# Optimization experiments

Hardware: AMD Instinct MI355X
Metric: run time of the kernel (lower is better)

Reference implementation:

```python
import jax, jax.numpy as jnp
import numpy as np

EPS = 1e-5

def _layer_norm(x, w):
    mu = jnp.mean(x, axis=-1, keepdims=True)
    var = jnp.mean(jnp.square(x - mu), axis=-1, keepdims=True)
    return (x - mu) * jax.lax.rsqrt(var + EPS) * w

def setup_inputs() -> dict:
    key = jax.random.key(0)
    ks = jax.random.split(key, 5)
    B, T, C, H = 2, 2048, 1024, 16
    std = 0.02
    return {
        "x": jax.random.normal(ks[0], (B, T, C), dtype=jnp.float32),
        "ln1_w": jnp.ones((C,), dtype=jnp.float32),
        "w_attn": jax.random.normal(ks[1], (C, 3 * C), dtype=jnp.float32) * std,
        "w_proj": jax.random.normal(ks[2], (C, C), dtype=jnp.float32) * std,
        "ln2_w": jnp.ones((C,), dtype=jnp.float32),
        "w_fc": jax.random.normal(ks[3], (C, 4 * C), dtype=jnp.float32) * std,
        "w_cproj": jax.random.normal(ks[4], (4 * C, C), dtype=jnp.float32) * std,
    }

def reference(x, ln1_w, w_attn, w_proj, ln2_w, w_fc, w_cproj):
    B, T, C = x.shape
    H = 16
    Dh = C // H
    # --- causal self-attention on ln1(x) ---
    h = _layer_norm(x, ln1_w)
    qkv = h @ w_attn                      # [B,T,3C]
    q, k, v = jnp.split(qkv, 3, axis=-1)
    # [B,T,C] -> [B,H,T,Dh]
    q = q.reshape(B, T, H, Dh).transpose(0, 2, 1, 3)
    k = k.reshape(B, T, H, Dh).transpose(0, 2, 1, 3)
    v = v.reshape(B, T, H, Dh).transpose(0, 2, 1, 3)
    # NOTE: original scales by full embed dim C**-0.5, not head_dim**-0.5
    scores = jnp.einsum('bhqd,bhkd->bhqk', q, k) * (C ** -0.5)
    causal = jnp.tril(jnp.ones((T, T), dtype=bool))
    scores = jnp.where(causal, scores, -jnp.inf)
    probs = jax.nn.softmax(scores, axis=-1)  # dropout=0.0 (eval)
    y = jnp.einsum('bhqk,bhkd->bhqd', probs, v)
    y = y.transpose(0, 2, 1, 3).reshape(B, T, C)
    x = x + y @ w_proj
    # --- MLP on ln2(x) ---
    h = _layer_norm(x, ln2_w)
    x = x + jax.nn.relu(h @ w_fc) @ w_cproj
    return x
```

## Files before the change

### kernel.cpp

```cpp
#include <hip/hip_runtime.h>

typedef __attribute__((ext_vector_type(8))) __bf16 bf16x8;
typedef __attribute__((ext_vector_type(4))) float f32x4;
typedef __attribute__((ext_vector_type(8))) unsigned short u16x8;
typedef __attribute__((ext_vector_type(4))) unsigned short u16x4;
typedef unsigned short u16;

__device__ __forceinline__ u16 f2bf(float f) {
  return __builtin_bit_cast(u16, (__bf16)f);
}
__device__ __forceinline__ float bf2f(u16 u) {
  return __builtin_bit_cast(float, ((unsigned)u) << 16);
}

__device__ __forceinline__ f32x4 mfma16(bf16x8 a, bf16x8 b, f32x4 c) {
  return __builtin_amdgcn_mfma_f32_16x16x32_bf16(a, b, c, 0, 0, 0);
}

__device__ __forceinline__ void gl_lds16(const void* g, void* l) {
  __builtin_amdgcn_global_load_lds(
      (const __attribute__((address_space(1))) unsigned int*)g,
      (__attribute__((address_space(3))) unsigned int*)l, 16, 0, 0);
}

__device__ __forceinline__ f32x4 fmax4(f32x4 a, f32x4 b) {
  f32x4 r;
  r[0] = fmaxf(a[0], b[0]); r[1] = fmaxf(a[1], b[1]);
  r[2] = fmaxf(a[2], b[2]); r[3] = fmaxf(a[3], b[3]);
  return r;
}

__global__ __launch_bounds__(256) void convT_all(const float* __restrict__ w0,
                                                 u16* __restrict__ o0,
                                                 const float* __restrict__ w1,
                                                 u16* __restrict__ o1,
                                                 const float* __restrict__ w2,
                                                 u16* __restrict__ o2) {
  __shared__ float tile[64][65];
  const int id = blockIdx.x;
  const float* in;
  u16* outT;
  int K, N, bx, by;
  if (id < 768) { in = w0; outT = o0; K = 1024; N = 3072; bx = id & 15; by = id >> 4; }
  else if (id < 1024) { const int j = id - 768; in = w1; outT = o1; K = 1024; N = 1024; bx = j & 15; by = j >> 4; }
  else { const int j = id - 1024; in = w2; outT = o2; K = 1024; N = 4096; bx = j & 15; by = j >> 4; }
  const int t = threadIdx.x;
  const int tk = bx * 64, tn = by * 64;
  const int lk = t >> 4, ln = (t & 15) * 4;
#pragma unroll
  for (int r = 0; r < 4; ++r) {
    const int k = lk + r * 16;
    const float4 v = *(const float4*)(in + (size_t)(tk + k) * N + tn + ln);
    tile[k][ln + 0] = v.x; tile[k][ln + 1] = v.y;
    tile[k][ln + 2] = v.z; tile[k][ln + 3] = v.w;
  }
  __syncthreads();
  const int sn = t >> 2, sk = (t & 3) * 4;
#pragma unroll
  for (int j = 0; j < 4; ++j) {
    const int k = sk + j * 16;
    ushort4 o;
    o.x = f2bf(tile[k + 0][sn]); o.y = f2bf(tile[k + 1][sn]);
    o.z = f2bf(tile[k + 2][sn]); o.w = f2bf(tile[k + 3][sn]);
    *(ushort4*)(outT + (size_t)(tn + sn) * K + tk + k) = o;
  }
}

__global__ __launch_bounds__(256) void convT(const float* __restrict__ in,
                                             u16* __restrict__ outT, int K, int N) {
  __shared__ float tile[64][65];
  const int t = threadIdx.x;
  const int tk = blockIdx.x * 64, tn = blockIdx.y * 64;
  const int lk = t >> 4, ln = (t & 15) * 4;
#pragma unroll
  for (int r = 0; r < 4; ++r) {
    const int k = lk + r * 16;
    const float4 v = *(const float4*)(in + (size_t)(tk + k) * N + tn + ln);
    tile[k][ln + 0] = v.x; tile[k][ln + 1] = v.y;
    tile[k][ln + 2] = v.z; tile[k][ln + 3] = v.w;
  }
  __syncthreads();
  const int sn = t >> 2, sk = (t & 3) * 4;
#pragma unroll
  for (int j = 0; j < 4; ++j) {
    const int k = sk + j * 16;
    ushort4 o;
    o.x = f2bf(tile[k + 0][sn]); o.y = f2bf(tile[k + 1][sn]);
    o.z = f2bf(tile[k + 2][sn]); o.w = f2bf(tile[k + 3][sn]);
    *(ushort4*)(outT + (size_t)(tn + sn) * K + tk + k) = o;
  }
}

__global__ __launch_bounds__(256) void vtrans(const u16* __restrict__ qkvb,
                                              u16* __restrict__ vT) {
  __shared__ u16 tile[64][72];
  const int t = threadIdx.x;
  const int tt0 = blockIdx.x * 64;
  const int bh = blockIdx.y;
  const int b = bh >> 4, h = bh & 15;
  const u16* src = qkvb + (size_t)(b * 2048 + tt0) * 3072 + 2048 + h * 64;
  {
    const int tl = t >> 2, d0 = (t & 3) * 16;
    const u16x8 a0 = *(const u16x8*)(src + (size_t)tl * 3072 + d0);
    const u16x8 a1 = *(const u16x8*)(src + (size_t)tl * 3072 + d0 + 8);
    *(u16x8*)(&tile[tl][d0]) = a0;
    *(u16x8*)(&tile[tl][d0 + 8]) = a1;
  }
  __syncthreads();
  {
    const int dh = t >> 2, t0 = (t & 3) * 16;
    u16x8 o0, o1;
#pragma unroll
    for (int jj = 0; jj < 8; ++jj) {
      o0[jj] = tile[t0 + jj][dh];
      o1[jj] = tile[t0 + 8 + jj][dh];
    }
    u16* dst = vT + ((size_t)bh * 64 + dh) * 2048 + tt0 + t0;
    *(u16x8*)dst = o0;
    *(u16x8*)(dst + 8) = o1;
  }
}

__global__ __launch_bounds__(256) void ln_bf16(const float* __restrict__ x,
                                               const float* __restrict__ wgt,
                                               u16* __restrict__ out) {
  const int row = blockIdx.x, t = threadIdx.x;
  const float4 v = ((const float4*)(x + (size_t)row * 1024))[t];
  float s = v.x + v.y + v.z + v.w;
  float q = v.x * v.x + v.y * v.y + v.z * v.z + v.w * v.w;
#pragma unroll
  for (int d = 32; d; d >>= 1) { s += __shfl_xor(s, d); q += __shfl_xor(q, d); }
  __shared__ float sb[8];
  const int wv = t >> 6;
  if ((t & 63) == 0) { sb[wv] = s; sb[4 + wv] = q; }
  __syncthreads();
  s = sb[0] + sb[1] + sb[2] + sb[3];
  q = sb[4] + sb[5] + sb[6] + sb[7];
  const float mu = s * (1.f / 1024.f);
  const float rstd = rsqrtf(q * (1.f / 1024.f) - mu * mu + 1e-5f);
  const float4 w4 = ((const float4*)wgt)[t];
  ushort4 o;
  o.x = f2bf((v.x - mu) * rstd * w4.x);
  o.y = f2bf((v.y - mu) * rstd * w4.y);
  o.z = f2bf((v.z - mu) * rstd * w4.z);
  o.w = f2bf((v.w - mu) * rstd * w4.w);
  *(ushort4*)(out + (size_t)row * 1024 + t * 4) = o;
}

__global__ __launch_bounds__(256) void reduce_ln(const float* __restrict__ x,
                                                 const u16* __restrict__ p, int nseg,
                                                 const float* __restrict__ wgt,
                                                 float* __restrict__ x1,
                                                 u16* __restrict__ h2) {
  const int row = blockIdx.x, t = threadIdx.x;
  const size_t ro = (size_t)row * 1024 + t * 4;
  float4 v = *(const float4*)(x + ro);
  for (int sgm = 0; sgm < nseg; ++sgm) {
    const ushort4 u = *(const ushort4*)(p + (size_t)sgm * 4096 * 1024 + ro);
    v.x += bf2f(u.x); v.y += bf2f(u.y); v.z += bf2f(u.z); v.w += bf2f(u.w);
  }
  *(float4*)(x1 + ro) = v;
  float s = v.x + v.y + v.z + v.w;
  float q = v.x * v.x + v.y * v.y + v.z * v.z + v.w * v.w;
#pragma unroll
  for (int d = 32; d; d >>= 1) { s += __shfl_xor(s, d); q += __shfl_xor(q, d); }
  __shared__ float sb[8];
  const int wv = t >> 6;
  if ((t & 63) == 0) { sb[wv] = s; sb[4 + wv] = q; }
  __syncthreads();
  s = sb[0] + sb[1] + sb[2] + sb[3];
  q = sb[4] + sb[5] + sb[6] + sb[7];
  const float mu = s * (1.f / 1024.f);
  const float rstd = rsqrtf(q * (1.f / 1024.f) - mu * mu + 1e-5f);
  const float4 w4 = ((const float4*)wgt)[t];
  ushort4 o;
  o.x = f2bf((v.x - mu) * rstd * w4.x);
  o.y = f2bf((v.y - mu) * rstd * w4.y);
  o.z = f2bf((v.z - mu) * rstd * w4.z);
  o.w = f2bf((v.w - mu) * rstd * w4.w);
  *(ushort4*)(h2 + ro) = o;
}

__global__ __launch_bounds__(256) void reduce_out(const float* __restrict__ x1,
                                                  const u16* __restrict__ p, int nseg,
                                                  float* __restrict__ out) {
  const int i = blockIdx.x * blockDim.x + threadIdx.x;
  const size_t ro = (size_t)i * 4;
  float4 v = *(const float4*)(x1 + ro);
  for (int sgm = 0; sgm < nseg; ++sgm) {
    const ushort4 u = *(const ushort4*)(p + (size_t)sgm * 4096 * 1024 + ro);
    v.x += bf2f(u.x); v.y += bf2f(u.y); v.z += bf2f(u.z); v.w += bf2f(u.w);
  }
  *(float4*)(out + ro) = v;
}

template <int EPI>
__global__ __launch_bounds__(256) void gemm128(const u16* __restrict__ A,
                                               const u16* __restrict__ Bt,
                                               void* __restrict__ outp,
                                               int M, int N, int K) {
  __shared__ u16 As[2][4096];
  __shared__ u16 Bs[2][4096];
  const unsigned gx = gridDim.x, gy = gridDim.y, gxy = gx * gy;
  const unsigned nwg = gxy * gridDim.z;
  unsigned f = (blockIdx.z * gy + blockIdx.y) * gx + blockIdx.x;
  if ((nwg & 7u) == 0u) { const unsigned qq = nwg >> 3; f = (f & 7u) * qq + (f >> 3); }
  const int bx = f % gx, by = (f / gx) % gy, bz = f / gxy;

  const int t = threadIdx.x, w = t >> 6, l = t & 63;
  const int lr = l & 15, g = l >> 4;
  const int row0 = by * 128, col0 = bx * 128;
  const int segK = K / gridDim.z;
  const int k0 = bz * segK, kend = k0 + segK;
  const int wr = w >> 1, wc = w & 1;
  f32x4 acc[4][4] = {};

  const int sr = t >> 2;
  const int sk = (((t & 3) ^ (sr & 3)) << 3);
  const u16* Ag = A + (size_t)(row0 + sr) * K + sk;
  const u16* Bg = Bt + (size_t)(col0 + sr) * K + sk;
  const size_t rstride = (size_t)64 * K;

  auto stage = [&](int kt, int bb) {
    u16* AsW = As[bb] + w * 512;
    u16* BsW = Bs[bb] + w * 512;
    gl_lds16(Ag + kt, AsW);
    gl_lds16(Ag + kt + rstride, AsW + 2048);
    gl_lds16(Bg + kt, BsW);
    gl_lds16(Bg + kt + rstride, BsW + 2048);
  };

  const int gsw = (g ^ (lr & 3)) * 8;

  stage(k0, 0);
  __syncthreads();
  int cur = 0;
  for (int kt = k0; kt < kend; kt += 32) {
    if (kt + 32 < kend) stage(kt + 32, cur ^ 1);
    bf16x8 af[4], bfr[4];
#pragma unroll
    for (int m = 0; m < 4; ++m)
      af[m] = *(const bf16x8*)(As[cur] + (wr * 64 + m * 16 + lr) * 32 + gsw);
#pragma unroll
    for (int n = 0; n < 4; ++n)
      bfr[n] = *(const bf16x8*)(Bs[cur] + (wc * 64 + n * 16 + lr) * 32 + gsw);
#pragma unroll
    for (int m = 0; m < 4; ++m)
#pragma unroll
      for (int n = 0; n < 4; ++n) acc[m][n] = mfma16(af[m], bfr[n], acc[m][n]);
    __syncthreads();
    cur ^= 1;
  }

  const size_t segoff = (size_t)bz * M * N;
#pragma unroll
  for (int m = 0; m < 4; ++m)
#pragma unroll
    for (int n = 0; n < 4; ++n)
#pragma unroll
      for (int r = 0; r < 4; ++r) {
        const int row = row0 + wr * 64 + m * 16 + g * 4 + r;
        const int col = col0 + wc * 64 + n * 16 + lr;
        const size_t idx = (size_t)row * N + col;
        const float v = acc[m][n][r];
        if constexpr (EPI == 0) ((u16*)outp)[idx] = f2bf(v);
        else if constexpr (EPI == 2) ((u16*)outp)[idx] = f2bf(fmaxf(v, 0.f));
        else ((u16*)outp)[segoff + idx] = f2bf(v);
      }
}

template <int EPI>
__global__ __launch_bounds__(512, 2) void gemm256(const u16* __restrict__ A,
                                                  const u16* __restrict__ Bt,
                                                  u16* __restrict__ outp,
                                                  int M, int N, int K) {
  __shared__ u16 S[2][32768];
  const unsigned gx = gridDim.x, gy = gridDim.y, gxy = gx * gy;
  const unsigned nwg = gxy * gridDim.z;
  unsigned f = (blockIdx.z * gy + blockIdx.y) * gx + blockIdx.x;
  if ((nwg & 7u) == 0u) { const unsigned qq = nwg >> 3; f = (f & 7u) * qq + (f >> 3); }
  const int bx = f % gx, by = (f / gx) % gy, bz = f / gxy;
  const int t = threadIdx.x, w = t >> 6, l = t & 63;
  const int lr = l & 15, g = l >> 4;
  const int wr = w >> 2, wc = w & 3;
  const int row0 = by * 256, col0 = bx * 256;
  const int segK = K / gridDim.z;
  const int k0 = bz * segK;
  const int NT = segK >> 6;

  f32x4 acc[8][4] = {};

  const int jr0 = t >> 2;
  const int jr1 = jr0 + 128;
  const int jks = ((t & 3) ^ (jr0 & 3)) << 3;
  auto stage_half = [&](int ht, int idx) {
    const int buf = ht & 1;
    u16* db = &S[buf][(idx & 1) * 16384 + (idx >> 1) * 8192 + w * 512];
    const u16* gb = (idx & 1) ? Bt : A;
    const int rc0 = (idx & 1) ? col0 : row0;
    const int kb = k0 + ht * 64 + (idx >> 1) * 32;
    gl_lds16(gb + (size_t)(rc0 + jr0) * K + kb + jks, db);
    gl_lds16(gb + (size_t)(rc0 + jr1) * K + kb + jks, db + 4096);
  };

  const int gsw = (g ^ (lr & 3)) * 8;

  stage_half(0, 0); stage_half(0, 1); stage_half(0, 2); stage_half(0, 3);
  stage_half(1, 0); stage_half(1, 1);
  asm volatile("s_waitcnt vmcnt(4)" ::: "memory");
  __builtin_amdgcn_s_barrier();

  for (int T = 0; T < NT; ++T) {
    const int cur = T & 1;
    const u16* Ab = &S[cur][0];
    const u16* Bb = &S[cur][16384];
    bf16x8 bfr[4];
#pragma unroll
    for (int sub = 0; sub < 4; ++sub) {
      const int mq = sub & 1, ks = sub >> 1;
      if (mq == 0) {
#pragma unroll
        for (int n = 0; n < 4; ++n)
          bfr[n] = *(const bf16x8*)(Bb + ks * 8192 + (wc * 64 + n * 16 + lr) * 32 + gsw);
      }
      bf16x8 af[4];
#pragma unroll
      for (int m = 0; m < 4; ++m)
        af[m] = *(const bf16x8*)(Ab + ks * 8192 +
                                 (wr * 128 + mq * 64 + m * 16 + lr) * 32 + gsw);
      if (sub < 2) { if (T + 1 < NT) stage_half(T + 1, 2 + sub); }
      else         { if (T + 2 < NT) stage_half(T + 2, sub - 2); }
      __builtin_amdgcn_s_barrier();
      __builtin_amdgcn_s_setprio(1);
#pragma unroll
      for (int m = 0; m < 4; ++m)
#pragma unroll
        for (int n = 0; n < 4; ++n)
          acc[mq * 4 + m][n] = mfma16(af[m], bfr[n], acc[mq * 4 + m][n]);
      __builtin_amdgcn_s_setprio(0);
      if (sub == 3) asm volatile("s_waitcnt vmcnt(4)" ::: "memory");
      __builtin_amdgcn_s_barrier();
    }
  }

  const size_t segoff = (size_t)bz * M * N;
#pragma unroll
  for (int m = 0; m < 8; ++m)
#pragma unroll
    for (int n = 0; n < 4; ++n)
#pragma unroll
      for (int r = 0; r < 4; ++r) {
        const int row = row0 + wr * 128 + m * 16 + g * 4 + r;
        const int col = col0 + wc * 64 + n * 16 + lr;
        const size_t idx = (size_t)row * N + col;
        const float v = acc[m][n][r];
        if constexpr (EPI == 0) outp[idx] = f2bf(v);
        else if constexpr (EPI == 2) outp[idx] = f2bf(fmaxf(v, 0.f));
        else outp[segoff + idx] = f2bf(v);
      }
}

__global__ __launch_bounds__(256) void attn_fwd(const u16* __restrict__ qkvb,
                                                const u16* __restrict__ vT,
                                                u16* __restrict__ y) {
  __shared__ u16 Ks[2][4096];
  __shared__ u16 Vs[2][4096];
  __shared__ u16 Pb[4][16 * 64];
  const int t = threadIdx.x, w = t >> 6, l = t & 63;
  const int lr = l & 15, g = l >> 4;
  const unsigned f = blockIdx.y * gridDim.x + blockIdx.x;
  const int xcd = f & 7, j = f >> 3;
  const int bh = xcd + 8 * (j & 3);
  const int qt = 31 - (j >> 2);
  const int b = bh >> 4, h = bh & 15;
  const size_t base = (size_t)b * 2048 * 3072;
  const u16* Kg = qkvb + base + 1024 + h * 64;
  const u16* Vg = vT + (size_t)bh * 64 * 2048;
  u16* Pw = &Pb[w][0];
  const int pkey = (lr & 7) << 3;
  const float SCL = 0.0450842200277855f;

  auto stageK = [&](int kv0, int bb) {
#pragma unroll
    for (int r = 0; r < 2; ++r) {
      const int dl = (r * 256 + t) * 16;
      const int row = dl >> 7;
      const int srcb = (dl & 127) ^ ((row & 7) << 4);
      gl_lds16(Kg + (size_t)(kv0 + row) * 3072 + (srcb >> 1),
               (char*)Ks[bb] + r * 4096 + w * 1024);
    }
  };
  auto stageV = [&](int kv0, int bb) {
#pragma unroll
    for (int r = 0; r < 2; ++r) {
      const int dl = (r * 256 + t) * 16;
      const int dh = dl >> 7;
      const int srcb = (dl & 127) ^ ((dh & 7) << 4);
      gl_lds16(Vg + (size_t)dh * 2048 + kv0 + (srcb >> 1),
               (char*)Vs[bb] + r * 4096 + w * 1024);
    }
  };

  const int q0w = qt * 64 + w * 16, nt = qt + 1;
  const u16* Qp = qkvb + base + (size_t)(q0w + lr) * 3072 + h * 64;
  const bf16x8 qf0 = *(const bf16x8*)(Qp + g * 8);
  const bf16x8 qf1 = *(const bf16x8*)(Qp + 32 + g * 8);
  f32x4 o[4] = {};
  float m1 = -1e30f, s1 = 0.f;

  stageK(0, 0);
  stageV(0, 0);
  __syncthreads();

  int ct = 0;
  for (int tt = 0; tt < nt; ++tt) {
    const int kv0 = tt * 64;
    if (tt + 1 < nt) {
      stageK(kv0 + 64, ct ^ 1);
      stageV(kv0 + 64, ct ^ 1);
    }

    const u16* Kbuf = Ks[ct];
    const u16* Vbuf = Vs[ct];
    f32x4 s4[4];
#pragma unroll
    for (int i = 0; i < 4; ++i) {
      const int row = i * 16 + lr;
      const int sw = (row & 7) << 4;
      const bf16x8 k0 = *(const bf16x8*)(Kbuf + row * 64 + (((g * 16) ^ sw) >> 1));
      const bf16x8 k1 = *(const bf16x8*)(Kbuf + row * 64 + (((64 + g * 16) ^ sw) >> 1));
      f32x4 z = {0.f, 0.f, 0.f, 0.f};
      z = mfma16(k0, qf0, z);
      s4[i] = mfma16(k1, qf1, z);
    }
    if (kv0 + 64 > q0w) {
#pragma unroll
      for (int i = 0; i < 4; ++i)
#pragma unroll
        for (int r = 0; r < 4; ++r)
          if (kv0 + i * 16 + g * 4 + r > q0w + lr) s4[i][r] = -1e30f;
    }
    const f32x4 mm = fmax4(fmax4(s4[0], s4[1]), fmax4(s4[2], s4[3]));
    float mx = fmaxf(fmaxf(mm[0], mm[1]), fmaxf(mm[2], mm[3]));
    mx = fmaxf(mx, __shfl_xor(mx, 16));
    mx = fmaxf(mx, __shfl_xor(mx, 32));
    const float mxs = mx * SCL;
    if (!__all(mxs <= m1 + 8.f)) {
      const float mn = fmaxf(m1, mxs);
      const float sc = exp2f(m1 - mn);
      m1 = mn;
      s1 *= sc;
      float scr[4];
#pragma unroll
      for (int r = 0; r < 4; ++r) scr[r] = __shfl(sc, g * 4 + r);
#pragma unroll
      for (int n = 0; n < 4; ++n)
#pragma unroll
        for (int r = 0; r < 4; ++r) o[n][r] *= scr[r];
    }
    float ps = 0.f;
#pragma unroll
    for (int i = 0; i < 4; ++i) {
      u16x4 pk;
#pragma unroll
      for (int r = 0; r < 4; ++r) {
        const float p = exp2f(fmaf(s4[i][r], SCL, -m1));
        ps += p;
        pk[r] = f2bf(p);
      }
      *(u16x4*)(Pw + lr * 64 + ((i * 16 + g * 4) ^ pkey)) = pk;
    }
    s1 += ps;
#pragma unroll
    for (int s = 0; s < 2; ++s) {
      const bf16x8 pa = *(const bf16x8*)(Pw + lr * 64 + ((s * 32 + g * 8) ^ pkey));
#pragma unroll
      for (int n = 0; n < 4; ++n) {
        const int dh = n * 16 + lr;
        const bf16x8 vf = *(const bf16x8*)(
            Vbuf + dh * 64 + (((s * 64 + g * 16) ^ ((dh & 7) << 4)) >> 1));
        o[n] = mfma16(pa, vf, o[n]);
      }
    }
    __syncthreads();
    ct ^= 1;
  }

  float den = s1;
  den += __shfl_xor(den, 16);
  den += __shfl_xor(den, 32);
  const float iv = 1.f / den;
  float ivr[4];
#pragma unroll
  for (int r = 0; r < 4; ++r) ivr[r] = __shfl(iv, g * 4 + r);
#pragma unroll
  for (int n = 0; n < 4; ++n)
#pragma unroll
    for (int r = 0; r < 4; ++r) {
      const int row = q0w + g * 4 + r;
      const int col = h * 64 + n * 16 + lr;
      y[(size_t)(b * 2048 + row) * 1024 + col] = f2bf(o[n][r] * ivr[r]);
    }
}

extern "C" void kernel_launch(void* const* d_in, const int* in_sizes, int n_in,
                              void* d_out, int out_size, void* d_ws, size_t ws_size,
                              hipStream_t stream) {
  const float* x      = (const float*)d_in[0];
  const float* ln1w   = (const float*)d_in[1];
  const float* wattn  = (const float*)d_in[2];
  const float* wproj  = (const float*)d_in[3];
  const float* ln2w   = (const float*)d_in[4];
  const float* wfc    = (const float*)d_in[5];
  const float* wcproj = (const float*)d_in[6];
  float* out = (float*)d_out;
  char* ws = (char*)d_ws;
  const size_t MB = 1024 * 1024;
  u16* qkvb    = (u16*)(ws + 0);
  u16* projP   = (u16*)(ws + 0);
  u16* cprojP  = (u16*)(ws + 0);
  u16* h1      = (u16*)(ws + 24 * MB);
  float* x1    = (float*)(ws + 48 * MB);
  u16* yb      = (u16*)(ws + 64 * MB);
  u16* h2      = (u16*)(ws + 64 * MB);
  u16* vT      = (u16*)(ws + 72 * MB);
  u16* hf      = (u16*)(ws + 72 * MB);
  u16* wattnT  = (u16*)(ws + 104 * MB);
  u16* wprojT  = (u16*)(ws + 110 * MB);
  u16* wcprojT = (u16*)(ws + 104 * MB);
  u16* wfcT    = (u16*)(ws + 112 * MB);

  convT_all<<<2048, 256, 0, stream>>>(wattn, wattnT, wproj, wprojT, wfc, wfcT);

  ln_bf16<<<4096, 256, 0, stream>>>(x, ln1w, h1);
  gemm256<0><<<dim3(12, 16, 1), 512, 0, stream>>>(h1, wattnT, qkvb, 4096, 3072, 1024);
  vtrans<<<dim3(32, 32), 256, 0, stream>>>(qkvb, vT);
  attn_fwd<<<dim3(32, 32), 256, 0, stream>>>(qkvb, vT, yb);
  gemm128<4><<<dim3(8, 32, 4), 256, 0, stream>>>(yb, wprojT, projP, 4096, 1024, 1024);
  convT<<<dim3(64, 16), 256, 0, stream>>>(wcproj, wcprojT, 4096, 1024);
  reduce_ln<<<4096, 256, 0, stream>>>(x, projP, 4, ln2w, x1, h2);
  gemm256<2><<<dim3(16, 16, 1), 512, 0, stream>>>(h2, wfcT, hf, 4096, 4096, 1024);
  gemm256<4><<<dim3(4, 16, 4), 512, 0, stream>>>(hf, wcprojT, cprojP, 4096, 1024, 4096);
  reduce_out<<<4096, 256, 0, stream>>>(x1, cprojP, 4, out);
}
```

Before: 230.8 us.

## Split long causal attention query tiles across two blocks with a combine kernel

Query tiles 15-31 now split their KV loop into two halves handled by separate blocks. Each half writes unnormalized fp32 partial outputs plus running max and denominator, and a new combine kernel merges them. The aim is to shorten the critical-path work of the longest causal tiles and balance load across CUs. In exchange it adds an extra launch and fp32 partial traffic through the workspace.

```diff
diff --git a/kernel.cpp b/kernel.cpp
--- a/kernel.cpp
+++ b/kernel.cpp
@@ -362,16 +362,25 @@
 
 __global__ __launch_bounds__(256) void attn_fwd(const u16* __restrict__ qkvb,
                                                 const u16* __restrict__ vT,
-                                                u16* __restrict__ y) {
+                                                u16* __restrict__ y,
+                                                float* __restrict__ po,
+                                                float* __restrict__ pm) {
   __shared__ u16 Ks[2][4096];
   __shared__ u16 Vs[2][4096];
   __shared__ u16 Pb[4][16 * 64];
   const int t = threadIdx.x, w = t >> 6, l = t & 63;
   const int lr = l & 15, g = l >> 4;
-  const unsigned f = blockIdx.y * gridDim.x + blockIdx.x;
+  const unsigned f = blockIdx.x;
   const int xcd = f & 7, j = f >> 3;
   const int bh = xcd + 8 * (j & 3);
-  const int qt = 31 - (j >> 2);
+  const int j2 = j >> 2;
+  int qt, seg, split;
+  if (j2 < 34) { qt = 31 - (j2 >> 1); seg = j2 & 1; split = 1; }
+  else { qt = 48 - j2; seg = 0; split = 0; }
+  const int nt0 = qt + 1;
+  const int half = (nt0 + 1) >> 1;
+  const int t_begin = (split && seg) ? half : 0;
+  const int t_end = (split && !seg) ? half : nt0;
   const int b = bh >> 4, h = bh & 15;
   const size_t base = (size_t)b * 2048 * 3072;
   const u16* Kg = qkvb + base + 1024 + h * 64;
@@ -401,21 +410,21 @@
     }
   };
 
-  const int q0w = qt * 64 + w * 16, nt = qt + 1;
+  const int q0w = qt * 64 + w * 16;
   const u16* Qp = qkvb + base + (size_t)(q0w + lr) * 3072 + h * 64;
   const bf16x8 qf0 = *(const bf16x8*)(Qp + g * 8);
   const bf16x8 qf1 = *(const bf16x8*)(Qp + 32 + g * 8);
   f32x4 o[4] = {};
   float m1 = -1e30f, s1 = 0.f;
 
-  stageK(0, 0);
-  stageV(0, 0);
+  stageK(t_begin * 64, 0);
+  stageV(t_begin * 64, 0);
   __syncthreads();
 
   int ct = 0;
-  for (int tt = 0; tt < nt; ++tt) {
+  for (int tt = t_begin; tt < t_end; ++tt) {
     const int kv0 = tt * 64;
-    if (tt + 1 < nt) {
+    if (tt + 1 < t_end) {
       stageK(kv0 + 64, ct ^ 1);
       stageV(kv0 + 64, ct ^ 1);
     }
@@ -489,18 +498,62 @@
   float den = s1;
   den += __shfl_xor(den, 16);
   den += __shfl_xor(den, 32);
-  const float iv = 1.f / den;
-  float ivr[4];
-#pragma unroll
-  for (int r = 0; r < 4; ++r) ivr[r] = __shfl(iv, g * 4 + r);
-#pragma unroll
-  for (int n = 0; n < 4; ++n)
-#pragma unroll
-    for (int r = 0; r < 4; ++r) {
-      const int row = q0w + g * 4 + r;
-      const int col = h * 64 + n * 16 + lr;
-      y[(size_t)(b * 2048 + row) * 1024 + col] = f2bf(o[n][r] * ivr[r]);
-    }
+
+  if (split) {
+    const int pidx = (bh * 17 + (qt - 15)) * 2 + seg;
+    float* pob = po + ((size_t)pidx * 64 + w * 16) * 64;
+#pragma unroll
+    for (int n = 0; n < 4; ++n)
+#pragma unroll
+      for (int r = 0; r < 4; ++r)
+        pob[(g * 4 + r) * 64 + n * 16 + lr] = o[n][r];
+    if (l < 16)
+      *(float2*)(pm + ((size_t)pidx * 64 + w * 16 + l) * 2) = make_float2(m1, den);
+  } else {
+    const float iv = 1.f / den;
+    float ivr[4];
+#pragma unroll
+    for (int r = 0; r < 4; ++r) ivr[r] = __shfl(iv, g * 4 + r);
+#pragma unroll
+    for (int n = 0; n < 4; ++n)
+#pragma unroll
+      for (int r = 0; r < 4; ++r) {
+        const int row = q0w + g * 4 + r;
+        const int col = h * 64 + n * 16 + lr;
+        y[(size_t)(b * 2048 + row) * 1024 + col] = f2bf(o[n][r] * ivr[r]);
+      }
+  }
+}
+
+__global__ __launch_bounds__(256) void attn_combine(const float* __restrict__ po,
+                                                    const float* __restrict__ pm,
+                                                    u16* __restrict__ y) {
+  const int c = blockIdx.x;
+  const int bh = c & 31, qti = c >> 5;
+  const int qt = 15 + qti;
+  const int b = bh >> 4, h = bh & 15;
+  const int t = threadIdx.x;
+  const int row = t >> 2, c0 = (t & 3) * 16;
+  const int pidx = (bh * 17 + qti) * 2;
+  const float2 ms0 = *(const float2*)(pm + ((size_t)(pidx + 0) * 64 + row) * 2);
+  const float2 ms1 = *(const float2*)(pm + ((size_t)(pidx + 1) * 64 + row) * 2);
+  const float mm = fmaxf(ms0.x, ms1.x);
+  const float w0 = exp2f(ms0.x - mm), w1 = exp2f(ms1.x - mm);
+  const float inv = 1.f / (ms0.y * w0 + ms1.y * w1);
+  const float* p0 = po + ((size_t)(pidx + 0) * 64 + row) * 64 + c0;
+  const float* p1 = po + ((size_t)(pidx + 1) * 64 + row) * 64 + c0;
+  u16* yp = y + (size_t)(b * 2048 + qt * 64 + row) * 1024 + h * 64 + c0;
+#pragma unroll
+  for (int jj = 0; jj < 4; ++jj) {
+    const float4 a = ((const float4*)p0)[jj];
+    const float4 bb = ((const float4*)p1)[jj];
+    ushort4 ov;
+    ov.x = f2bf((a.x * w0 + bb.x * w1) * inv);
+    ov.y = f2bf((a.y * w0 + bb.y * w1) * inv);
+    ov.z = f2bf((a.z * w0 + bb.z * w1) * inv);
+    ov.w = f2bf((a.w * w0 + bb.w * w1) * inv);
+    ((ushort4*)yp)[jj] = ov;
+  }
 }
 
 extern "C" void kernel_launch(void* const* d_in, const int* in_sizes, int n_in,
@@ -520,7 +573,9 @@
   u16* projP   = (u16*)(ws + 0);
   u16* cprojP  = (u16*)(ws + 0);
   u16* h1      = (u16*)(ws + 24 * MB);
+  float* po    = (float*)(ws + 32 * MB);
   float* x1    = (float*)(ws + 48 * MB);
+  float* pm    = (float*)(ws + 50 * MB);
   u16* yb      = (u16*)(ws + 64 * MB);
   u16* h2      = (u16*)(ws + 64 * MB);
   u16* vT      = (u16*)(ws + 72 * MB);
@@ -535,7 +590,8 @@
   ln_bf16<<<4096, 256, 0, stream>>>(x, ln1w, h1);
   gemm256<0><<<dim3(12, 16, 1), 512, 0, stream>>>(h1, wattnT, qkvb, 4096, 3072, 1024);
   vtrans<<<dim3(32, 32), 256, 0, stream>>>(qkvb, vT);
-  attn_fwd<<<dim3(32, 32), 256, 0, stream>>>(qkvb, vT, yb);
+  attn_fwd<<<1568, 256, 0, stream>>>(qkvb, vT, yb, po, pm);
+  attn_combine<<<544, 256, 0, stream>>>(po, pm, yb);
   gemm128<4><<<dim3(8, 32, 4), 256, 0, stream>>>(yb, wprojT, projP, 4096, 1024, 1024);
   convT<<<dim3(64, 16), 256, 0, stream>>>(wcproj, wcprojT, 4096, 1024);
   reduce_ln<<<4096, 256, 0, stream>>>(x, projP, 4, ln2w, x1, h2);
```

Result: no change. 232.9 us (+0.9%).
